# Kernel optimization log

Hardware: AMD Instinct MI355X
Metric: run time of the kernel (lower is better)

## Reference

```python
import jax, jax.numpy as jnp
import numpy as np

EMBED_DIM = 512
N_QUBITS = 8


def setup_inputs() -> dict:
    key = jax.random.key(0)
    k_x, k_rot, k_ent = jax.random.split(key, 3)
    x = jax.random.normal(k_x, (8, 2048, EMBED_DIM), dtype=jnp.float32)
    rotation = jax.random.normal(k_rot, (EMBED_DIM, N_QUBITS), dtype=jnp.float32)
    entangle = jax.random.normal(k_ent, (N_QUBITS - 1,), dtype=jnp.float32)  # unused in fwd, kept for parity
    return {"x": x, "rotation": rotation, "entangle": entangle}


def reference(x, rotation, entangle):
    # rot: (B, L, Q)
    rot = jnp.einsum('ble,ej->blj', x, rotation)
    # pairwise dot products: (B, L, L) == the python double loop fused into one matmul
    probs = jax.nn.sigmoid(jnp.einsum('biq,bjq->bij', rot, rot))
    scores = probs / jnp.sum(probs, axis=-1, keepdims=True)
    return scores
```

## Files before the change

kernel.cpp:

```cpp
#include <hip/hip_runtime.h>
#include <math.h>

#define EMBED 512
#define NQ 8
#define SEQ 2048
#define NB 8
#define LOG2E 1.4426950408889634f

typedef float vfloat4 __attribute__((ext_vector_type(4)));

#define RPAD 516

__global__ __launch_bounds__(256) void qa_rot(
    const float* __restrict__ x, const float* __restrict__ R,
    float* __restrict__ rotT) {
    __shared__ float rt[NQ * RPAD];
#pragma unroll
    for (int m = 0; m < (EMBED * NQ) / 256; ++m) {
        int f = threadIdx.x + m * 256;
        rt[(f & 7) * RPAD + (f >> 3)] = R[f];
    }
    __syncthreads();

    const int q = threadIdx.x & 7;
    const int rslot = threadIdx.x >> 3;
    const int b = blockIdx.x >> 6;
    const int i = ((blockIdx.x & 63) << 5) + rslot;

    const vfloat4* __restrict__ xr =
        (const vfloat4*)(x + ((size_t)b * SEQ + i) * EMBED);
    const vfloat4* __restrict__ rr = (const vfloat4*)(rt + q * RPAD);

    vfloat4 acc = {0.f, 0.f, 0.f, 0.f};
#pragma unroll 8
    for (int m = 0; m < EMBED / 4; ++m) {
        acc += xr[m] * rr[m];
    }
    rotT[(size_t)b * (NQ * SEQ) + (size_t)q * SEQ + i] =
        (acc.x + acc.y) + (acc.z + acc.w);
}

#define K2_THREADS 512
#define TI 2
#define ROWS_PER_BLOCK 16

__global__ __launch_bounds__(K2_THREADS, 4) void qa_scores(
    const float* __restrict__ rotT, float* __restrict__ out) {
    __shared__ float lds[NQ * SEQ];
    const int b = blockIdx.x >> 7;
    const int i0blk = (blockIdx.x & 127) * ROWS_PER_BLOCK;
    const float* __restrict__ rt = rotT + (size_t)b * (NQ * SEQ);

    {
        const vfloat4* __restrict__ src = (const vfloat4*)rt;
        vfloat4* dst = (vfloat4*)lds;
#pragma unroll
        for (int m = 0; m < (NQ * SEQ / 4) / K2_THREADS; ++m)
            dst[threadIdx.x + m * K2_THREADS] = src[threadIdx.x + m * K2_THREADS];
    }
    __syncthreads();

    const int wave = threadIdx.x >> 6;
    const int lane = threadIdx.x & 63;
    const int i0 = i0blk + wave * TI;

    float ri[TI][NQ];
#pragma unroll
    for (int r = 0; r < TI; ++r)
#pragma unroll
        for (int q = 0; q < NQ; ++q)
            ri[r][q] = lds[q * SEQ + i0 + r];

    vfloat4 pv[8][TI];
    float rsum[TI] = {0.f, 0.f};

#pragma unroll
    for (int t = 0; t < 8; ++t) {
        vfloat4 s[TI];
#pragma unroll
        for (int r = 0; r < TI; ++r) s[r] = (vfloat4){0.f, 0.f, 0.f, 0.f};
#pragma unroll
        for (int q = 0; q < NQ; ++q) {
            vfloat4 rj = *((const vfloat4*)(lds + q * SEQ + t * 256) + lane);
#pragma unroll
            for (int r = 0; r < TI; ++r)
                s[r] += rj * ri[r][q];
        }
#pragma unroll
        for (int r = 0; r < TI; ++r) {
            vfloat4 p;
            p.x = __builtin_amdgcn_rcpf(1.f + __builtin_amdgcn_exp2f(-s[r].x * LOG2E));
            p.y = __builtin_amdgcn_rcpf(1.f + __builtin_amdgcn_exp2f(-s[r].y * LOG2E));
            p.z = __builtin_amdgcn_rcpf(1.f + __builtin_amdgcn_exp2f(-s[r].z * LOG2E));
            p.w = __builtin_amdgcn_rcpf(1.f + __builtin_amdgcn_exp2f(-s[r].w * LOG2E));
            pv[t][r] = p;
            rsum[r] += (p.x + p.y) + (p.z + p.w);
        }
    }

#pragma unroll
    for (int r = 0; r < TI; ++r) {
#pragma unroll
        for (int off = 32; off > 0; off >>= 1)
            rsum[r] += __shfl_xor(rsum[r], off);
        rsum[r] = __builtin_amdgcn_rcpf(rsum[r]);
    }

#pragma unroll
    for (int r = 0; r < TI; ++r) {
        float* __restrict__ orow = out + ((size_t)b * SEQ + i0 + r) * SEQ;
#pragma unroll
        for (int t = 0; t < 8; ++t) {
            vfloat4 v = pv[t][r] * rsum[r];
            __builtin_nontemporal_store(v, (vfloat4*)(orow + t * 256) + lane);
        }
    }
}

extern "C" void kernel_launch(void* const* d_in, const int* in_sizes, int n_in,
                              void* d_out, int out_size, void* d_ws, size_t ws_size,
                              hipStream_t stream) {
    const float* x        = (const float*)d_in[0];
    const float* rotation = (const float*)d_in[1];
    float* out = (float*)d_out;

    float* rotT = (float*)d_ws;

    qa_rot<<<NB * 64, 256, 0, stream>>>(x, rotation, rotT);
    qa_scores<<<NB * 128, K2_THREADS, 0, stream>>>(rotT, out);
}
```

Before: 171.3 us.

## Recompute sigmoid in second pass instead of holding probabilities; double rows per block

The scores kernel no longer keeps all sigmoid values in registers between the row-sum pass and the store pass. It recomputes the dot products and sigmoids in a second sweep over LDS, which frees registers. The saved registers pay for four rows per wave instead of two, so there are half as many blocks and half as many redundant LDS fills of the rotation table. The cost is roughly double the exp/rcp and FMA work per output element, while the kernel remains dominated by output writes.

```diff
diff --git a/kernel.cpp b/kernel.cpp
--- a/kernel.cpp
+++ b/kernel.cpp
@@ -41,14 +41,23 @@
 }
 
 #define K2_THREADS 512
-#define TI 2
-#define ROWS_PER_BLOCK 16
+#define TI 4
+#define ROWS_PER_BLOCK 32
+
+__device__ __forceinline__ vfloat4 sigmoid4(vfloat4 s) {
+    vfloat4 p;
+    p.x = __builtin_amdgcn_rcpf(1.f + __builtin_amdgcn_exp2f(-s.x * LOG2E));
+    p.y = __builtin_amdgcn_rcpf(1.f + __builtin_amdgcn_exp2f(-s.y * LOG2E));
+    p.z = __builtin_amdgcn_rcpf(1.f + __builtin_amdgcn_exp2f(-s.z * LOG2E));
+    p.w = __builtin_amdgcn_rcpf(1.f + __builtin_amdgcn_exp2f(-s.w * LOG2E));
+    return p;
+}
 
 __global__ __launch_bounds__(K2_THREADS, 4) void qa_scores(
     const float* __restrict__ rotT, float* __restrict__ out) {
     __shared__ float lds[NQ * SEQ];
-    const int b = blockIdx.x >> 7;
-    const int i0blk = (blockIdx.x & 127) * ROWS_PER_BLOCK;
+    const int b = blockIdx.x >> 6;
+    const int i0blk = (blockIdx.x & 63) * ROWS_PER_BLOCK;
     const float* __restrict__ rt = rotT + (size_t)b * (NQ * SEQ);
 
     {
@@ -71,9 +80,7 @@
         for (int q = 0; q < NQ; ++q)
             ri[r][q] = lds[q * SEQ + i0 + r];
 
-    vfloat4 pv[8][TI];
-    float rsum[TI] = {0.f, 0.f};
-
+    float rsum[TI] = {0.f, 0.f, 0.f, 0.f};
 #pragma unroll
     for (int t = 0; t < 8; ++t) {
         vfloat4 s[TI];
@@ -88,31 +95,38 @@
         }
 #pragma unroll
         for (int r = 0; r < TI; ++r) {
-            vfloat4 p;
-            p.x = __builtin_amdgcn_rcpf(1.f + __builtin_amdgcn_exp2f(-s[r].x * LOG2E));
-            p.y = __builtin_amdgcn_rcpf(1.f + __builtin_amdgcn_exp2f(-s[r].y * LOG2E));
-            p.z = __builtin_amdgcn_rcpf(1.f + __builtin_amdgcn_exp2f(-s[r].z * LOG2E));
-            p.w = __builtin_amdgcn_rcpf(1.f + __builtin_amdgcn_exp2f(-s[r].w * LOG2E));
-            pv[t][r] = p;
+            vfloat4 p = sigmoid4(s[r]);
             rsum[r] += (p.x + p.y) + (p.z + p.w);
         }
     }
 
+    float rinv[TI];
 #pragma unroll
     for (int r = 0; r < TI; ++r) {
 #pragma unroll
         for (int off = 32; off > 0; off >>= 1)
             rsum[r] += __shfl_xor(rsum[r], off);
-        rsum[r] = __builtin_amdgcn_rcpf(rsum[r]);
+        rinv[r] = __builtin_amdgcn_rcpf(rsum[r]);
     }
 
+    float* __restrict__ orow0 = out + ((size_t)b * SEQ + i0) * SEQ;
 #pragma unroll
-    for (int r = 0; r < TI; ++r) {
-        float* __restrict__ orow = out + ((size_t)b * SEQ + i0 + r) * SEQ;
+    for (int t = 0; t < 8; ++t) {
+        vfloat4 s[TI];
 #pragma unroll
-        for (int t = 0; t < 8; ++t) {
-            vfloat4 v = pv[t][r] * rsum[r];
-            __builtin_nontemporal_store(v, (vfloat4*)(orow + t * 256) + lane);
+        for (int r = 0; r < TI; ++r) s[r] = (vfloat4){0.f, 0.f, 0.f, 0.f};
+#pragma unroll
+        for (int q = 0; q < NQ; ++q) {
+            vfloat4 rj = *((const vfloat4*)(lds + q * SEQ + t * 256) + lane);
+#pragma unroll
+            for (int r = 0; r < TI; ++r)
+                s[r] += rj * ri[r][q];
+        }
+#pragma unroll
+        for (int r = 0; r < TI; ++r) {
+            vfloat4 v = sigmoid4(s[r]) * rinv[r];
+            __builtin_nontemporal_store(
+                v, (vfloat4*)(orow0 + (size_t)r * SEQ + t * 256) + lane);
         }
     }
 }
@@ -127,5 +141,5 @@
     float* rotT = (float*)d_ws;
 
     qa_rot<<<NB * 64, 256, 0, stream>>>(x, rotation, rotT);
-    qa_scores<<<NB * 128, K2_THREADS, 0, stream>>>(rotT, out);
+    qa_scores<<<NB * 64, K2_THREADS, 0, stream>>>(rotT, out);
 }
```

After: 172.6 us. About the same (+0.8%).
